# Kernel tuning notes

Measured on AMD Instinct MI355X. Metric: run time of the kernel, lower is better.

The kernel has to match this reference:

```python
import jax, jax.numpy as jnp
import numpy as np

B, N, C = 8, 4096, 768
NUM_HEADS = 8
HEAD_DIM = C // NUM_HEADS
FOCUSING_FACTOR = 3


def setup_inputs() -> dict:
    key = jax.random.key(0)
    ks = jax.random.split(key, 8)
    x = jax.random.normal(ks[0], (B, N, C), dtype=jnp.float32)
    Wq = jax.random.normal(ks[1], (C, C), dtype=jnp.float32) * 0.02
    Wkv = jax.random.normal(ks[2], (C, C), dtype=jnp.float32) * 0.02
    Wproj = jax.random.normal(ks[3], (C, C), dtype=jnp.float32) * 0.02
    bproj = jnp.zeros((C,), dtype=jnp.float32)
    w_g = jax.random.normal(ks[4], (C, 1), dtype=jnp.float32)
    # scale / positional_encoding are zero-init Parameters; use small random
    # values so the numerics are non-trivial for kernel testing.
    scale_p = jax.random.normal(ks[5], (1, 1, C), dtype=jnp.float32) * 0.02
    pos_enc = jax.random.normal(ks[6], (1, N, C), dtype=jnp.float32) * 0.02
    return {"x": x, "H": 64, "W": 64, "Wq": Wq, "Wkv": Wkv,
            "Wproj": Wproj, "bproj": bproj, "w_g": w_g,
            "scale_p": scale_p, "pos_enc": pos_enc}


def _l2norm(v, axis):
    return jnp.sqrt(jnp.sum(v * v, axis=axis, keepdims=True))


def reference(x, H, W, Wq, Wkv, Wproj, bproj, w_g, scale_p, pos_enc):
    Bx, Nx, Cx = x.shape
    scale_factor = HEAD_DIM ** (-0.5)
    q = jnp.einsum('bnc,dc->bnd', x, Wq)      # (B,N,C)
    k = jnp.einsum('bnc,dc->bnd', x, Wkv)     # kv -> k
    # global aggregation weight
    A = (q @ w_g) * scale_factor              # (B,N,1)
    A = A / jnp.maximum(_l2norm(A, axis=1), 1e-12)  # F.normalize over dim=1
    G = jnp.sum(A * q, axis=1)                # (B,C)
    xg = G[:, None, :] * k                    # (B,N,C)
    k = k + pos_enc
    # focusing feature map
    scale = jax.nn.softplus(scale_p)
    q = (jax.nn.relu(q) + 1e-6) / scale
    k = (jax.nn.relu(k) + 1e-6) / scale
    q_norm = _l2norm(q, axis=-1)
    k_norm = _l2norm(k, axis=-1)
    q = q ** FOCUSING_FACTOR
    k = k ** FOCUSING_FACTOR
    q = q / _l2norm(q, axis=-1) * q_norm
    k = k / _l2norm(k, axis=-1) * k_norm
    # split heads: (B, H, N, d)
    q = q.reshape(Bx, Nx, NUM_HEADS, HEAD_DIM).transpose(0, 2, 1, 3)
    k = k.reshape(Bx, Nx, NUM_HEADS, HEAD_DIM).transpose(0, 2, 1, 3)
    k_mean = k.mean(axis=2)                   # (B,H,d)
    z = 1.0 / (jnp.einsum('bhnd,bhd->bhn', q, k_mean)[..., None] + 1e-6)
    xg = xg.reshape(Bx, Nx, NUM_HEADS, HEAD_DIM).transpose(0, 2, 1, 3)
    xg = xg * z                               # (B,H,N,d)
    out = xg.transpose(0, 2, 1, 3).reshape(Bx, Nx, Cx)
    out = jnp.einsum('bnc,dc->bnd', out, Wproj) + bproj
    return out
```

## Files before the change

### kernel.cpp

```cpp
#include <hip/hip_runtime.h>
#include <hip/hip_bf16.h>
#include <cstdint>
#include <cstddef>


#define GLOAD_LDS16(g, l) \
  __builtin_amdgcn_global_load_lds((const __attribute__((address_space(1))) void*)(g), \
                                   (__attribute__((address_space(3))) void*)(l), 16, 0, 0)

typedef __attribute__((ext_vector_type(8))) short bf16x8;
typedef __attribute__((ext_vector_type(4))) float f32x4;

__device__ __forceinline__ ushort f2bf(float f) {
  union { float f; uint32_t u; } v; v.f = f;
  uint32_t u = v.u;
  uint32_t r = u + 0x7fffu + ((u >> 16) & 1u);
  return (ushort)(r >> 16);
}

__global__ __launch_bounds__(256) void k_conv(const float* __restrict__ src,
                                              ushort* __restrict__ dst, int n4) {
  int i = blockIdx.x * blockDim.x + threadIdx.x;
  int stride = gridDim.x * blockDim.x;
  for (; i < n4; i += stride) {
    float4 v = ((const float4*)src)[i];
    ushort4 o;
    o.x = f2bf(v.x); o.y = f2bf(v.y); o.z = f2bf(v.z); o.w = f2bf(v.w);
    ((ushort4*)dst)[i] = o;
  }
}

__global__ void k_softplus(const float* __restrict__ p, float* __restrict__ sinv) {
  int i = threadIdx.x + blockIdx.x * 256;
  if (i < 768) {
    float x = p[i];
    float s = (x > 20.f) ? x : log1pf(expf(x));
    sinv[i] = 1.0f / s;
  }
}

__global__ __launch_bounds__(256, 2) void gemm_bt(
    const ushort* __restrict__ A, const ushort* __restrict__ Bt,
    float* __restrict__ C, const float* __restrict__ bias, int Ncols) {
  constexpr int K = 768, BK = 64;
  __shared__ ushort lA[128 * BK];
  __shared__ ushort lB[128 * BK];
  const int tid  = threadIdx.x;
  const int lane = tid & 63;
  const int w    = tid >> 6;
  const int wr   = w >> 1, wc = w & 1;
  const int m0 = blockIdx.y * 128;
  const int n0 = blockIdx.x * 128;
  const int sr = lane >> 3;
  const int sc = (lane & 7) * 8;

  f32x4 acc[4][4] = {};

  for (int kt = 0; kt < K / BK; ++kt) {
    const int k0 = kt * BK;
    __syncthreads();
#pragma unroll
    for (int i = 0; i < 4; ++i) {
      const int ci = w * 4 + i;
      const int r  = ci * 8 + sr;
      GLOAD_LDS16(A  + (size_t)(m0 + r) * K + (k0 + sc), lA + ci * 512);
      GLOAD_LDS16(Bt + (size_t)(n0 + r) * K + (k0 + sc), lB + ci * 512);
    }
    __syncthreads();
#pragma unroll
    for (int kk = 0; kk < BK / 32; ++kk) {
      bf16x8 af[4], bfr[4];
#pragma unroll
      for (int m = 0; m < 4; ++m)
        af[m] = *(const bf16x8*)&lA[(wr * 64 + m * 16 + (lane & 15)) * BK + kk * 32 + (lane >> 4) * 8];
#pragma unroll
      for (int n = 0; n < 4; ++n)
        bfr[n] = *(const bf16x8*)&lB[(wc * 64 + n * 16 + (lane & 15)) * BK + kk * 32 + (lane >> 4) * 8];
#pragma unroll
      for (int m = 0; m < 4; ++m)
#pragma unroll
        for (int n = 0; n < 4; ++n)
          acc[m][n] = __builtin_amdgcn_mfma_f32_16x16x32_bf16(af[m], bfr[n], acc[m][n], 0, 0, 0);
    }
  }
#pragma unroll
  for (int n = 0; n < 4; ++n) {
    const int col = n0 + wc * 64 + n * 16 + (lane & 15);
    const float bv = bias ? bias[col] : 0.0f;
#pragma unroll
    for (int m = 0; m < 4; ++m) {
      const int row0 = m0 + wr * 64 + m * 16 + (lane >> 4) * 4;
#pragma unroll
      for (int j = 0; j < 4; ++j)
        C[(size_t)(row0 + j) * Ncols + col] = acc[m][n][j] + bv;
    }
  }
}

__global__ __launch_bounds__(256) void k_arow(const float* __restrict__ qk,
                                              const float* __restrict__ wg,
                                              float* __restrict__ A_raw,
                                              float* __restrict__ bsumsq) {
  __shared__ float lwg[768];
  __shared__ float lsq[4];
  const int tid = threadIdx.x, lane = tid & 63, w = tid >> 6;
  for (int i = tid; i < 768; i += 256) lwg[i] = wg[i];
  __syncthreads();
  const float sf = 0.10206207261596575f;
  float wsq = 0.f;
  for (int r8 = 0; r8 < 8; ++r8) {
    const int row = blockIdx.x * 32 + w * 8 + r8;
    const float* qr = qk + (size_t)row * 1536;
    float d = 0.f;
#pragma unroll
    for (int i = 0; i < 12; ++i) d += qr[lane + 64 * i] * lwg[lane + 64 * i];
#pragma unroll
    for (int m = 32; m; m >>= 1) d += __shfl_xor(d, m);
    d *= sf;
    if (lane == 0) { A_raw[row] = d; wsq += d * d; }
  }
  if (lane == 0) lsq[w] = wsq;
  __syncthreads();
  if (tid == 0) atomicAdd(&bsumsq[blockIdx.x >> 7], lsq[0] + lsq[1] + lsq[2] + lsq[3]);
}

__global__ void k_rnorm(const float* __restrict__ bsumsq, float* __restrict__ rnorm) {
  int t = threadIdx.x;
  if (t < 8) rnorm[t] = 1.0f / fmaxf(sqrtf(bsumsq[t]), 1e-12f);
}

__global__ __launch_bounds__(256) void k_gks(const float* __restrict__ qk,
                                             const float* __restrict__ pos,
                                             const float* __restrict__ A_raw,
                                             const float* __restrict__ rnorm,
                                             const float* __restrict__ sinv,
                                             float* __restrict__ part) {
  __shared__ float pG[4][768];
  __shared__ float pK[4][768];
  const int tid = threadIdx.x, lane = tid & 63, w = tid >> 6;
  const int b = blockIdx.x >> 7;
  const int c0 = lane * 12;
  float sv[12], ga[12] = {}, ka[12] = {};
#pragma unroll
  for (int v = 0; v < 3; ++v) {
    float4 s = *(const float4*)(sinv + c0 + v * 4);
    sv[v * 4] = s.x; sv[v * 4 + 1] = s.y; sv[v * 4 + 2] = s.z; sv[v * 4 + 3] = s.w;
  }
  const float rb = rnorm[b];
  for (int r = 0; r < 8; ++r) {
    const int row = blockIdx.x * 32 + w * 8 + r;
    const float* qr = qk + (size_t)row * 1536;
    const float* pr = pos + (size_t)(row & 4095) * 768;
    float q[12], kk[12], u[12];
    float s1 = 0.f, s2 = 0.f;
#pragma unroll
    for (int v = 0; v < 3; ++v) {
      float4 qv = *(const float4*)(qr + c0 + v * 4);
      float4 kv = *(const float4*)(qr + 768 + c0 + v * 4);
      float4 pv = *(const float4*)(pr + c0 + v * 4);
      q[v * 4] = qv.x; q[v * 4 + 1] = qv.y; q[v * 4 + 2] = qv.z; q[v * 4 + 3] = qv.w;
      kk[v * 4] = kv.x + pv.x; kk[v * 4 + 1] = kv.y + pv.y;
      kk[v * 4 + 2] = kv.z + pv.z; kk[v * 4 + 3] = kv.w + pv.w;
    }
#pragma unroll
    for (int j = 0; j < 12; ++j) {
      float t = (fmaxf(kk[j], 0.f) + 1e-6f) * sv[j];
      float uu = t * t * t;
      u[j] = uu;
      s1 += t * t; s2 += uu * uu;
    }
#pragma unroll
    for (int m = 32; m; m >>= 1) { s1 += __shfl_xor(s1, m); s2 += __shfl_xor(s2, m); }
    const float ratio = sqrtf(s1 / s2);
    const float a = A_raw[row] * rb;
#pragma unroll
    for (int j = 0; j < 12; ++j) { ka[j] += u[j] * ratio; ga[j] += a * q[j]; }
  }
#pragma unroll
  for (int j = 0; j < 12; ++j) { pG[w][c0 + j] = ga[j]; pK[w][c0 + j] = ka[j]; }
  __syncthreads();
  float* outp = part + (size_t)blockIdx.x * 1536;
  for (int i = tid; i < 768; i += 256) {
    outp[i]       = pG[0][i] + pG[1][i] + pG[2][i] + pG[3][i];
    outp[768 + i] = pK[0][i] + pK[1][i] + pK[2][i] + pK[3][i];
  }
}

__global__ __launch_bounds__(256) void k_gred(const float* __restrict__ part,
                                              float* __restrict__ G,
                                              float* __restrict__ ksum) {
  const int i = blockIdx.x * 256 + threadIdx.x;
  const int b = blockIdx.y;
  const float* p = part + (size_t)b * 128 * 1536 + i;
  float s = 0.f;
#pragma unroll 8
  for (int blk = 0; blk < 128; ++blk) s += p[(size_t)blk * 1536];
  if (i < 768) G[b * 768 + i] = s;
  else         ksum[b * 768 + i - 768] = s;
}

__global__ __launch_bounds__(256) void k_y(const float* __restrict__ qk,
                                           const float* __restrict__ G,
                                           const float* __restrict__ ksum,
                                           const float* __restrict__ sinv,
                                           ushort* __restrict__ y) {
  const int tid = threadIdx.x, lane = tid & 63, w = tid >> 6;
  const int row = blockIdx.x * 4 + w;
  const int b = row >> 12;
  const int c0 = lane * 12;
  const float* qr = qk + (size_t)row * 1536;
  float q[12], kk[12], u[12], ks[12], gg[12];
  float s1 = 0.f, s2 = 0.f;
#pragma unroll
  for (int v = 0; v < 3; ++v) {
    float4 qv = *(const float4*)(qr + c0 + v * 4);
    float4 kv = *(const float4*)(qr + 768 + c0 + v * 4);
    float4 sv = *(const float4*)(sinv + c0 + v * 4);
    float4 kv2 = *(const float4*)(ksum + b * 768 + c0 + v * 4);
    float4 gv = *(const float4*)(G + b * 768 + c0 + v * 4);
#pragma unroll
    for (int e = 0; e < 4; ++e) {
      const int j = v * 4 + e;
      const float qe = (&qv.x)[e];
      q[j] = qe; kk[j] = (&kv.x)[e];
      float t = (fmaxf(qe, 0.f) + 1e-6f) * (&sv.x)[e];
      float uu = t * t * t;
      u[j] = uu; s1 += t * t; s2 += uu * uu;
      ks[j] = (&kv2.x)[e]; gg[j] = (&gv.x)[e];
    }
  }
#pragma unroll
  for (int m = 32; m; m >>= 1) { s1 += __shfl_xor(s1, m); s2 += __shfl_xor(s2, m); }
  const float ratio = sqrtf(s1 / s2);
  float zp = 0.f;
#pragma unroll
  for (int j = 0; j < 12; ++j) zp += u[j] * ks[j];
  zp += __shfl_xor(zp, 1); zp += __shfl_xor(zp, 2); zp += __shfl_xor(zp, 4);
  const float z = 1.0f / (ratio * zp * (1.0f / 4096.0f) + 1e-6f);
  ushort o[12];
#pragma unroll
  for (int j = 0; j < 12; ++j) o[j] = f2bf(gg[j] * kk[j] * z);
  ushort* yp = y + (size_t)row * 768 + c0;
#pragma unroll
  for (int v = 0; v < 3; ++v)
    *(ushort4*)(yp + v * 4) = *(ushort4*)(o + v * 4);
}

extern "C" void kernel_launch(void* const* d_in, const int* in_sizes, int n_in,
                              void* d_out, int out_size, void* d_ws, size_t ws_size,
                              hipStream_t stream) {
  const float* x      = (const float*)d_in[0];
  const float* Wq     = (const float*)d_in[3];
  const float* Wkv    = (const float*)d_in[4];
  const float* Wproj  = (const float*)d_in[5];
  const float* bproj  = (const float*)d_in[6];
  const float* wg     = (const float*)d_in[7];
  const float* scalep = (const float*)d_in[8];
  const float* pos    = (const float*)d_in[9];

  char* ws = (char*)d_ws;
  float*  qk   = (float*)ws;
  ushort* xbf  = (ushort*)(ws + 201326592);
  ushort* ybf  = xbf;
  float*  part = (float*)(ws + 201326592);
  ushort* wqk  = (ushort*)(ws + 251658240);
  ushort* wpj  = (ushort*)(ws + 254017536);
  float*  sinv = (float*)(ws + 255197184);
  float*  araw = (float*)(ws + 255200256);
  float*  acc  = (float*)(ws + 255331328);
  float* bsumsq = acc;
  float* Gv     = acc + 8;
  float* ksum   = acc + 8 + 6144;
  float* rnorm  = acc + 8 + 12288;

  hipMemsetAsync(bsumsq, 0, 8 * sizeof(float), stream);

  k_conv<<<4096, 256, 0, stream>>>(x, xbf, 25165824 / 4);
  k_conv<<<576, 256, 0, stream>>>(Wq, wqk, 589824 / 4);
  k_conv<<<576, 256, 0, stream>>>(Wkv, wqk + 589824, 589824 / 4);
  k_conv<<<576, 256, 0, stream>>>(Wproj, wpj, 589824 / 4);
  k_softplus<<<3, 256, 0, stream>>>(scalep, sinv);

  gemm_bt<<<dim3(12, 256), 256, 0, stream>>>(xbf, wqk, qk, nullptr, 1536);

  k_arow<<<1024, 256, 0, stream>>>(qk, wg, araw, bsumsq);
  k_rnorm<<<1, 64, 0, stream>>>(bsumsq, rnorm);
  k_gks<<<1024, 256, 0, stream>>>(qk, pos, araw, rnorm, sinv, part);
  k_gred<<<dim3(6, 8), 256, 0, stream>>>(part, Gv, ksum);
  k_y<<<8192, 256, 0, stream>>>(qk, Gv, ksum, sinv, ybf);

  gemm_bt<<<dim3(6, 256), 256, 0, stream>>>(ybf, wpj, (float*)d_out, bproj, 768);
}
```

Measured before the change: 486.4 us.

## Store QK projection in bf16 and fold A-row dot into key-sum kernel

The first GEMM now writes its q/k output as bf16 instead of fp32, which halves the intermediate traffic that the later passes read. The separate A-row kernel, its atomic accumulation and the memset are removed. The w_g dot product is computed inside k_gks, which accumulates unnormalized G plus per-block sums of squares. A small reduction kernel then derives the per-batch normalizer, and that scale is applied in k_gred. The trade-off is bf16 rounding of q/k, which adds precision loss in the cubic focusing and normalization steps.

New measurement: 423.6 us. 1.15x faster.

```diff
diff --git a/kernel.cpp b/kernel.cpp
--- a/kernel.cpp
+++ b/kernel.cpp
@@ -13,9 +13,11 @@
 
 __device__ __forceinline__ ushort f2bf(float f) {
   union { float f; uint32_t u; } v; v.f = f;
-  uint32_t u = v.u;
-  uint32_t r = u + 0x7fffu + ((u >> 16) & 1u);
+  uint32_t r = v.u + 0x7fffu + ((v.u >> 16) & 1u);
   return (ushort)(r >> 16);
+}
+__device__ __forceinline__ float bf2f(ushort u) {
+  union { uint32_t x; float f; } v; v.x = (uint32_t)u << 16; return v.f;
 }
 
 __global__ __launch_bounds__(256) void k_conv(const float* __restrict__ src,
@@ -39,9 +41,10 @@
   }
 }
 
+template <bool BF16OUT>
 __global__ __launch_bounds__(256, 2) void gemm_bt(
     const ushort* __restrict__ A, const ushort* __restrict__ Bt,
-    float* __restrict__ C, const float* __restrict__ bias, int Ncols) {
+    void* __restrict__ Cv, const float* __restrict__ bias, int Ncols) {
   constexpr int K = 768, BK = 64;
   __shared__ ushort lA[128 * BK];
   __shared__ ushort lB[128 * BK];
@@ -86,107 +89,105 @@
 #pragma unroll
   for (int n = 0; n < 4; ++n) {
     const int col = n0 + wc * 64 + n * 16 + (lane & 15);
-    const float bv = bias ? bias[col] : 0.0f;
+    const float bv = (!BF16OUT && bias) ? bias[col] : 0.0f;
 #pragma unroll
     for (int m = 0; m < 4; ++m) {
       const int row0 = m0 + wr * 64 + m * 16 + (lane >> 4) * 4;
 #pragma unroll
-      for (int j = 0; j < 4; ++j)
-        C[(size_t)(row0 + j) * Ncols + col] = acc[m][n][j] + bv;
-    }
-  }
-}
-
-__global__ __launch_bounds__(256) void k_arow(const float* __restrict__ qk,
-                                              const float* __restrict__ wg,
-                                              float* __restrict__ A_raw,
-                                              float* __restrict__ bsumsq) {
-  __shared__ float lwg[768];
+      for (int j = 0; j < 4; ++j) {
+        if (BF16OUT)
+          ((ushort*)Cv)[(size_t)(row0 + j) * Ncols + col] = f2bf(acc[m][n][j]);
+        else
+          ((float*)Cv)[(size_t)(row0 + j) * Ncols + col] = acc[m][n][j] + bv;
+      }
+    }
+  }
+}
+
+__global__ __launch_bounds__(256) void k_gks(const ushort* __restrict__ qk,
+                                             const float* __restrict__ pos,
+                                             const float* __restrict__ wg,
+                                             const float* __restrict__ sinv,
+                                             float* __restrict__ part,
+                                             float* __restrict__ partW) {
+  __shared__ float pG[4][768];
+  __shared__ float pK[4][768];
   __shared__ float lsq[4];
   const int tid = threadIdx.x, lane = tid & 63, w = tid >> 6;
-  for (int i = tid; i < 768; i += 256) lwg[i] = wg[i];
-  __syncthreads();
-  const float sf = 0.10206207261596575f;
-  float wsq = 0.f;
-  for (int r8 = 0; r8 < 8; ++r8) {
-    const int row = blockIdx.x * 32 + w * 8 + r8;
-    const float* qr = qk + (size_t)row * 1536;
-    float d = 0.f;
-#pragma unroll
-    for (int i = 0; i < 12; ++i) d += qr[lane + 64 * i] * lwg[lane + 64 * i];
-#pragma unroll
-    for (int m = 32; m; m >>= 1) d += __shfl_xor(d, m);
-    d *= sf;
-    if (lane == 0) { A_raw[row] = d; wsq += d * d; }
-  }
-  if (lane == 0) lsq[w] = wsq;
-  __syncthreads();
-  if (tid == 0) atomicAdd(&bsumsq[blockIdx.x >> 7], lsq[0] + lsq[1] + lsq[2] + lsq[3]);
-}
-
-__global__ void k_rnorm(const float* __restrict__ bsumsq, float* __restrict__ rnorm) {
-  int t = threadIdx.x;
-  if (t < 8) rnorm[t] = 1.0f / fmaxf(sqrtf(bsumsq[t]), 1e-12f);
-}
-
-__global__ __launch_bounds__(256) void k_gks(const float* __restrict__ qk,
-                                             const float* __restrict__ pos,
-                                             const float* __restrict__ A_raw,
-                                             const float* __restrict__ rnorm,
-                                             const float* __restrict__ sinv,
-                                             float* __restrict__ part) {
-  __shared__ float pG[4][768];
-  __shared__ float pK[4][768];
-  const int tid = threadIdx.x, lane = tid & 63, w = tid >> 6;
-  const int b = blockIdx.x >> 7;
   const int c0 = lane * 12;
-  float sv[12], ga[12] = {}, ka[12] = {};
+  float sv[12], wv[12], ga[12] = {}, ka[12] = {};
 #pragma unroll
   for (int v = 0; v < 3; ++v) {
     float4 s = *(const float4*)(sinv + c0 + v * 4);
-    sv[v * 4] = s.x; sv[v * 4 + 1] = s.y; sv[v * 4 + 2] = s.z; sv[v * 4 + 3] = s.w;
-  }
-  const float rb = rnorm[b];
+    float4 g = *(const float4*)(wg + c0 + v * 4);
+#pragma unroll
+    for (int e = 0; e < 4; ++e) { sv[v * 4 + e] = (&s.x)[e]; wv[v * 4 + e] = (&g.x)[e]; }
+  }
+  float wsq = 0.f;
   for (int r = 0; r < 8; ++r) {
     const int row = blockIdx.x * 32 + w * 8 + r;
-    const float* qr = qk + (size_t)row * 1536;
+    const ushort* qr = qk + (size_t)row * 1536;
     const float* pr = pos + (size_t)(row & 4095) * 768;
     float q[12], kk[12], u[12];
-    float s1 = 0.f, s2 = 0.f;
+    float d = 0.f, s1 = 0.f, s2 = 0.f;
 #pragma unroll
     for (int v = 0; v < 3; ++v) {
-      float4 qv = *(const float4*)(qr + c0 + v * 4);
-      float4 kv = *(const float4*)(qr + 768 + c0 + v * 4);
+      ushort4 qv = *(const ushort4*)(qr + c0 + v * 4);
+      ushort4 kv = *(const ushort4*)(qr + 768 + c0 + v * 4);
       float4 pv = *(const float4*)(pr + c0 + v * 4);
-      q[v * 4] = qv.x; q[v * 4 + 1] = qv.y; q[v * 4 + 2] = qv.z; q[v * 4 + 3] = qv.w;
-      kk[v * 4] = kv.x + pv.x; kk[v * 4 + 1] = kv.y + pv.y;
-      kk[v * 4 + 2] = kv.z + pv.z; kk[v * 4 + 3] = kv.w + pv.w;
+#pragma unroll
+      for (int e = 0; e < 4; ++e) {
+        const int j = v * 4 + e;
+        q[j] = bf2f((&qv.x)[e]);
+        kk[j] = bf2f((&kv.x)[e]) + (&pv.x)[e];
+      }
     }
 #pragma unroll
     for (int j = 0; j < 12; ++j) {
+      d += q[j] * wv[j];
       float t = (fmaxf(kk[j], 0.f) + 1e-6f) * sv[j];
       float uu = t * t * t;
       u[j] = uu;
       s1 += t * t; s2 += uu * uu;
     }
 #pragma unroll
-    for (int m = 32; m; m >>= 1) { s1 += __shfl_xor(s1, m); s2 += __shfl_xor(s2, m); }
+    for (int m = 32; m; m >>= 1) {
+      d += __shfl_xor(d, m); s1 += __shfl_xor(s1, m); s2 += __shfl_xor(s2, m);
+    }
     const float ratio = sqrtf(s1 / s2);
-    const float a = A_raw[row] * rb;
-#pragma unroll
-    for (int j = 0; j < 12; ++j) { ka[j] += u[j] * ratio; ga[j] += a * q[j]; }
+    wsq += d * d;
+#pragma unroll
+    for (int j = 0; j < 12; ++j) { ka[j] += u[j] * ratio; ga[j] += d * q[j]; }
   }
 #pragma unroll
   for (int j = 0; j < 12; ++j) { pG[w][c0 + j] = ga[j]; pK[w][c0 + j] = ka[j]; }
+  if (lane == 0) lsq[w] = wsq;
   __syncthreads();
   float* outp = part + (size_t)blockIdx.x * 1536;
   for (int i = tid; i < 768; i += 256) {
     outp[i]       = pG[0][i] + pG[1][i] + pG[2][i] + pG[3][i];
     outp[768 + i] = pK[0][i] + pK[1][i] + pK[2][i] + pK[3][i];
   }
+  if (tid == 0) partW[blockIdx.x] = lsq[0] + lsq[1] + lsq[2] + lsq[3];
+}
+
+__global__ __launch_bounds__(256) void k_rnorm(const float* __restrict__ partW,
+                                               float* __restrict__ rnorm) {
+  const int tid = threadIdx.x;
+  const int b = tid >> 5, j = tid & 31;
+  float s = 0.f;
+#pragma unroll
+  for (int v = 0; v < 4; ++v) s += partW[b * 128 + j * 4 + v];
+#pragma unroll
+  for (int m = 16; m; m >>= 1) s += __shfl_xor(s, m);
+  if (j == 0) {
+    const float sf = 0.10206207261596575f;
+    rnorm[b] = sf / fmaxf(sf * sqrtf(s), 1e-12f);
+  }
 }
 
 __global__ __launch_bounds__(256) void k_gred(const float* __restrict__ part,
+                                              const float* __restrict__ rnorm,
                                               float* __restrict__ G,
                                               float* __restrict__ ksum) {
   const int i = blockIdx.x * 256 + threadIdx.x;
@@ -195,11 +196,11 @@
   float s = 0.f;
 #pragma unroll 8
   for (int blk = 0; blk < 128; ++blk) s += p[(size_t)blk * 1536];
-  if (i < 768) G[b * 768 + i] = s;
+  if (i < 768) G[b * 768 + i] = s * rnorm[b];
   else         ksum[b * 768 + i - 768] = s;
 }
 
-__global__ __launch_bounds__(256) void k_y(const float* __restrict__ qk,
+__global__ __launch_bounds__(256) void k_y(const ushort* __restrict__ qk,
                                            const float* __restrict__ G,
                                            const float* __restrict__ ksum,
                                            const float* __restrict__ sinv,
@@ -208,22 +209,21 @@
   const int row = blockIdx.x * 4 + w;
   const int b = row >> 12;
   const int c0 = lane * 12;
-  const float* qr = qk + (size_t)row * 1536;
-  float q[12], kk[12], u[12], ks[12], gg[12];
+  const ushort* qr = qk + (size_t)row * 1536;
+  float kk[12], u[12], ks[12], gg[12];
   float s1 = 0.f, s2 = 0.f;
 #pragma unroll
   for (int v = 0; v < 3; ++v) {
-    float4 qv = *(const float4*)(qr + c0 + v * 4);
-    float4 kv = *(const float4*)(qr + 768 + c0 + v * 4);
+    ushort4 qv = *(const ushort4*)(qr + c0 + v * 4);
+    ushort4 kv = *(const ushort4*)(qr + 768 + c0 + v * 4);
     float4 sv = *(const float4*)(sinv + c0 + v * 4);
     float4 kv2 = *(const float4*)(ksum + b * 768 + c0 + v * 4);
     float4 gv = *(const float4*)(G + b * 768 + c0 + v * 4);
 #pragma unroll
     for (int e = 0; e < 4; ++e) {
       const int j = v * 4 + e;
-      const float qe = (&qv.x)[e];
-      q[j] = qe; kk[j] = (&kv.x)[e];
-      float t = (fmaxf(qe, 0.f) + 1e-6f) * (&sv.x)[e];
+      kk[j] = bf2f((&kv.x)[e]);
+      float t = (fmaxf(bf2f((&qv.x)[e]), 0.f) + 1e-6f) * (&sv.x)[e];
       float uu = t * t * t;
       u[j] = uu; s1 += t * t; s2 += uu * uu;
       ks[j] = (&kv2.x)[e]; gg[j] = (&gv.x)[e];
@@ -259,21 +259,18 @@
   const float* pos    = (const float*)d_in[9];
 
   char* ws = (char*)d_ws;
-  float*  qk   = (float*)ws;
-  ushort* xbf  = (ushort*)(ws + 201326592);
+  ushort* qk   = (ushort*)ws;
+  ushort* xbf  = (ushort*)(ws + 100663296);
   ushort* ybf  = xbf;
-  float*  part = (float*)(ws + 201326592);
-  ushort* wqk  = (ushort*)(ws + 251658240);
-  ushort* wpj  = (ushort*)(ws + 254017536);
-  float*  sinv = (float*)(ws + 255197184);
-  float*  araw = (float*)(ws + 255200256);
-  float*  acc  = (float*)(ws + 255331328);
-  float* bsumsq = acc;
-  float* Gv     = acc + 8;
-  float* ksum   = acc + 8 + 6144;
-  float* rnorm  = acc + 8 + 12288;
-
-  hipMemsetAsync(bsumsq, 0, 8 * sizeof(float), stream);
+  float*  part = (float*)(ws + 100663296);
+  ushort* wqk  = (ushort*)(ws + 150994944);
+  ushort* wpj  = (ushort*)(ws + 153354240);
+  float*  sinv = (float*)(ws + 154533888);
+  float*  partW = (float*)(ws + 154536960);
+  float*  accb  = (float*)(ws + 154541056);
+  float* Gv     = accb;
+  float* ksum   = accb + 6144;
+  float* rnorm  = accb + 12288;
 
   k_conv<<<4096, 256, 0, stream>>>(x, xbf, 25165824 / 4);
   k_conv<<<576, 256, 0, stream>>>(Wq, wqk, 589824 / 4);
@@ -281,13 +278,12 @@
   k_conv<<<576, 256, 0, stream>>>(Wproj, wpj, 589824 / 4);
   k_softplus<<<3, 256, 0, stream>>>(scalep, sinv);
 
-  gemm_bt<<<dim3(12, 256), 256, 0, stream>>>(xbf, wqk, qk, nullptr, 1536);
-
-  k_arow<<<1024, 256, 0, stream>>>(qk, wg, araw, bsumsq);
-  k_rnorm<<<1, 64, 0, stream>>>(bsumsq, rnorm);
-  k_gks<<<1024, 256, 0, stream>>>(qk, pos, araw, rnorm, sinv, part);
-  k_gred<<<dim3(6, 8), 256, 0, stream>>>(part, Gv, ksum);
+  gemm_bt<true><<<dim3(12, 256), 256, 0, stream>>>(xbf, wqk, qk, nullptr, 1536);
+
+  k_gks<<<1024, 256, 0, stream>>>(qk, pos, wg, sinv, part, partW);
+  k_rnorm<<<1, 256, 0, stream>>>(partW, rnorm);
+  k_gred<<<dim3(6, 8), 256, 0, stream>>>(part, rnorm, Gv, ksum);
   k_y<<<8192, 256, 0, stream>>>(qk, Gv, ksum, sinv, ybf);
 
-  gemm_bt<<<dim3(6, 256), 256, 0, stream>>>(ybf, wpj, (float*)d_out, bproj, 768);
-}
+  gemm_bt<false><<<dim3(6, 256), 256, 0, stream>>>(ybf, wpj, d_out, bproj, 768);
+}
```
